# Kernel optimization log

Measured on AMD Instinct MI355X. Metric: run time of the kernel, lower is better.

## Reference

```python
import jax, jax.numpy as jnp
import numpy as np
from jax import lax

# dims
B, T = 64, 1024
ANNOT, RNN, MEM, ATTN = 512, 1024, 512, 512
FILTERS, KSIZE = 32, 31
PAD = (KSIZE - 1) // 2  # 15, SAME padding


def setup_inputs() -> dict:
    key = jax.random.key(0)
    ks = jax.random.split(key, 20)
    s = 0.02
    return {
        "memory": jax.random.normal(ks[0], (B, MEM), jnp.float32),
        "context": jax.random.normal(ks[1], (B, ANNOT), jnp.float32),
        "rnn_state": jax.random.normal(ks[2], (B, RNN), jnp.float32),
        "annots": jax.random.normal(ks[3], (B, T, ANNOT), jnp.float32),
        "atten": jax.random.uniform(ks[4], (B, 2, T), jnp.float32),
        "mask": jnp.ones((B, T), jnp.int32),
        "t": 0,
        # GRUCell params (torch gate order: r, z, n)
        "W_ih": jax.random.normal(ks[5], (3 * RNN, ANNOT + MEM), jnp.float32) * s,
        "W_hh": jax.random.normal(ks[6], (3 * RNN, RNN), jnp.float32) * s,
        "b_ih": jnp.zeros((3 * RNN,), jnp.float32),
        "b_hh": jnp.zeros((3 * RNN,), jnp.float32),
        # location-sensitive attention params
        "conv_w": jax.random.normal(ks[7], (FILTERS, 2, KSIZE), jnp.float32) * s,
        "loc_w": jax.random.normal(ks[8], (ATTN, FILTERS), jnp.float32) * s,
        "loc_b": jnp.zeros((ATTN,), jnp.float32),
        "q_w": jax.random.normal(ks[9], (ATTN, RNN), jnp.float32) * s,
        "q_b": jnp.zeros((ATTN,), jnp.float32),
        "a_w": jax.random.normal(ks[10], (ATTN, ANNOT), jnp.float32) * s,
        "a_b": jnp.zeros((ATTN,), jnp.float32),
        "v_w": jax.random.normal(ks[11], (1, ATTN), jnp.float32) * s,
    }


def _gru_cell(x, h, W_ih, W_hh, b_ih, b_hh):
    gi = x @ W_ih.T + b_ih  # [B, 3H]
    gh = h @ W_hh.T + b_hh
    i_r, i_z, i_n = jnp.split(gi, 3, axis=-1)
    h_r, h_z, h_n = jnp.split(gh, 3, axis=-1)
    r = jax.nn.sigmoid(i_r + h_r)
    z = jax.nn.sigmoid(i_z + h_z)
    n = jnp.tanh(i_n + r * h_n)
    return (1.0 - z) * n + z * h


def reference(memory, context, rnn_state, annots, atten, mask, t,
              W_ih, W_hh, b_ih, b_hh, conv_w, loc_w, loc_b,
              q_w, q_b, a_w, a_b, v_w):
    # GRU step on [memory; prev_context]
    rnn_input = jnp.concatenate([memory, context], axis=-1)  # [B, MEM+ANNOT]
    rnn_output = _gru_cell(rnn_input, rnn_state, W_ih, W_hh, b_ih, b_hh)  # [B, RNN]

    # location features: SAME conv over [B, 2, T] -> [B, FILTERS, T]
    loc_conv = lax.conv_general_dilated(
        atten, conv_w, window_strides=(1,), padding=[(PAD, PAD)],
        dimension_numbers=("NCH", "OIH", "NCH"))
    processed_loc = jnp.einsum("bft,af->bta", loc_conv, loc_w) + loc_b  # [B,T,ATTN]

    processed_query = (rnn_output @ q_w.T + q_b)[:, None, :]            # [B,1,ATTN]
    processed_annots = jnp.einsum("btd,ad->bta", annots, a_w) + a_b     # [B,T,ATTN]

    energy = jnp.tanh(processed_query + processed_annots + processed_loc)
    alignment = jnp.einsum("bta,a->bt", energy, v_w[0])                 # [B,T]

    # mask fill with -inf where mask == 0
    alignment = jnp.where(mask == 0, -jnp.inf, alignment)

    # sigmoid-normalized attention weights
    sig = jax.nn.sigmoid(alignment)
    alignment = sig / jnp.sum(sig, axis=1, keepdims=True)               # [B,T]

    new_context = jnp.einsum("bt,btd->bd", alignment, annots)           # [B,ANNOT]
    return rnn_output, new_context, alignment
```

## Files before the change

kernel.cpp:

```cpp
#include <hip/hip_runtime.h>

typedef float f32x4 __attribute__((ext_vector_type(4)));
typedef short bf16x8 __attribute__((ext_vector_type(8)));

__device__ __forceinline__ unsigned int pk2(float a, float b) {
    unsigned int ua = __float_as_uint(a); ua += 0x7FFFu + ((ua >> 16) & 1u);
    unsigned int ub = __float_as_uint(b); ub += 0x7FFFu + ((ub >> 16) & 1u);
    return __builtin_amdgcn_perm(ub, ua, 0x07060302u);
}
__device__ __forceinline__ unsigned short bf16_rne(float a) {
    unsigned int ua = __float_as_uint(a);
    ua += 0x7FFFu + ((ua >> 16) & 1u);
    return (unsigned short)(ua >> 16);
}
__device__ __forceinline__ float tanh_fast(float x) {
    float e = __expf(x + x);
    return 1.f - 2.f / (e + 1.f);
}
__device__ __forceinline__ f32x4 mfma16(bf16x8 a, bf16x8 b, f32x4 c) {
    return __builtin_amdgcn_mfma_f32_16x16x32_bf16(a, b, c, 0, 0, 0);
}
__device__ __forceinline__ void ald16(const void* g, void* l) {
    __builtin_amdgcn_global_load_lds(
        (const __attribute__((address_space(1))) unsigned int*)g,
        (__attribute__((address_space(3))) unsigned int*)l, 16, 0, 0);
}

#define Q_WIH   786432
#define Q_WHH   1572864
#define Q_QW    1703936
#define Q_X2    1720320
#define Q_X1    1736704
#define Q_BAW   1802240
#define Q_BLW   1806336
#define Q_EB    1806464
#define NCVT    7057

__global__ __launch_bounds__(256) void k_prep(
    const float* __restrict__ Wih, const float* __restrict__ Whh,
    const float* __restrict__ qw, const float* __restrict__ rnn_state,
    const float* __restrict__ memory, const float* __restrict__ context,
    const float* __restrict__ aw, const float* __restrict__ lw,
    const float* __restrict__ ab, const float* __restrict__ lb,
    const float* __restrict__ atten, const float* __restrict__ convw,
    unsigned short* __restrict__ Wihb, unsigned short* __restrict__ Whhb,
    unsigned short* __restrict__ qwb, unsigned short* __restrict__ X2b,
    unsigned short* __restrict__ X1b, unsigned short* __restrict__ Bbig,
    float* __restrict__ ebias, unsigned short* __restrict__ Lconv)
{
    __shared__ float att_s[2 * 160];
    __shared__ float cw_s[1984];
    const int tid = threadIdx.x;
    if (blockIdx.x < NCVT) {
        int q = blockIdx.x * 256 + tid;
        if (q >= Q_EB) return;
        if (q < Q_WIH) {
            int i = q * 4;
            float4 v = *(const float4*)(Wih + i);
            uint2 u; u.x = pk2(v.x, v.y); u.y = pk2(v.z, v.w);
            *(uint2*)(Wihb + i) = u;
        } else if (q < Q_WHH) {
            int i = (q - Q_WIH) * 4;
            float4 v = *(const float4*)(Whh + i);
            uint2 u; u.x = pk2(v.x, v.y); u.y = pk2(v.z, v.w);
            *(uint2*)(Whhb + i) = u;
        } else if (q < Q_QW) {
            int i = (q - Q_WHH) * 4;
            float4 v = *(const float4*)(qw + i);
            uint2 u; u.x = pk2(v.x, v.y); u.y = pk2(v.z, v.w);
            *(uint2*)(qwb + i) = u;
        } else if (q < Q_X2) {
            int i = (q - Q_QW) * 4;
            float4 v = *(const float4*)(rnn_state + i);
            uint2 u; u.x = pk2(v.x, v.y); u.y = pk2(v.z, v.w);
            *(uint2*)(X2b + i) = u;
        } else if (q < Q_X1) {
            int i = (q - Q_X2) * 4;
            int b = i >> 10, c = i & 1023;
            const float* s = (c < 512) ? (memory + b * 512 + c) : (context + b * 512 + (c - 512));
            float4 v = *(const float4*)s;
            uint2 u; u.x = pk2(v.x, v.y); u.y = pk2(v.z, v.w);
            *(uint2*)(X1b + i) = u;
        } else if (q < Q_BAW) {
            int i = (q - Q_X1) * 4;
            int a = i >> 9, c = i & 511;
            float4 v = *(const float4*)(aw + a * 512 + c);
            uint2 u; u.x = pk2(v.x, v.y); u.y = pk2(v.z, v.w);
            *(uint2*)(Bbig + a * 544 + c) = u;
        } else if (q < Q_BLW) {
            int i = (q - Q_BAW) * 4;
            int a = i >> 5, c = i & 31;
            float4 v = *(const float4*)(lw + a * 32 + c);
            uint2 u; u.x = pk2(v.x, v.y); u.y = pk2(v.z, v.w);
            *(uint2*)(Bbig + a * 544 + 512 + c) = u;
        } else {
            int i = (q - Q_BLW) * 4;
            float4 va = *(const float4*)(ab + i);
            float4 vb = *(const float4*)(lb + i);
            float4 r; r.x = va.x + vb.x; r.y = va.y + vb.y; r.z = va.z + vb.z; r.w = va.w + vb.w;
            *(float4*)(ebias + i) = r;
        }
    } else {
        const int bid = blockIdx.x - NCVT;
        const int b = bid >> 3;
        const int tbase = (bid & 7) * 128;
        for (int i = tid; i < 320; i += 256) {
            int c = i / 160, j = i % 160;
            float v = 0.f;
            int pos = tbase - 15 + j;
            if (j < 158 && pos >= 0 && pos < 1024) v = atten[b * 2048 + c * 1024 + pos];
            att_s[c * 160 + j] = v;
        }
        for (int i = tid; i < 1984; i += 256) cw_s[i] = convw[i];
        __syncthreads();
        const int f = tid & 31, tq = tid >> 5;
        float acc[16];
#pragma unroll
        for (int i = 0; i < 16; ++i) acc[i] = 0.f;
        for (int c = 0; c < 2; ++c) {
            for (int k = 0; k < 31; ++k) {
                float w = cw_s[f * 62 + c * 31 + k];
                int base = c * 160 + tq * 16 + k;
#pragma unroll
                for (int ti = 0; ti < 16; ++ti) acc[ti] += w * att_s[base + ti];
            }
        }
#pragma unroll
        for (int ti = 0; ti < 16; ++ti) {
            int t = tbase + tq * 16 + ti;
            Lconv[(b * 1024 + t) * 32 + f] = bf16_rne(acc[ti]);
        }
    }
}

__global__ __launch_bounds__(256, 4) void k_gemm_ks(
    const unsigned short* __restrict__ A1, const unsigned short* __restrict__ A2,
    const unsigned short* __restrict__ B1, const unsigned short* __restrict__ B2,
    float* __restrict__ C, int N, int nTiles, int n_split, int K, int Klen)
{
    __shared__ __align__(16) unsigned short As[64 * 32];
    __shared__ __align__(16) unsigned short Bs[128 * 32];
    const int tid = threadIdx.x;
    const int nb = blockIdx.x % nTiles;
    const int ks = blockIdx.x / nTiles;
    const int nBase = nb * 128;
    const bool use2 = nBase >= n_split;
    const unsigned short* A = use2 ? A2 : A1;
    const unsigned short* B = use2 ? B2 : B1;
    const int brow0 = nBase - (use2 ? n_split : 0);
    const int lane = tid & 63, w = tid >> 6;
    const int c = lane & 15, qd = lane >> 4;
    const int lr = lane >> 2;
    const int swzl = ((lane & 3) ^ ((lr >> 1) & 3)) * 8;

    const f32x4 fz = {0.f, 0.f, 0.f, 0.f};
    f32x4 acc[4][2];
#pragma unroll
    for (int i = 0; i < 4; ++i) { acc[i][0] = fz; acc[i][1] = fz; }

    const int k0b = ks * Klen;
    const int nkc = Klen >> 5;
    for (int kc = 0; kc < nkc; ++kc) {
        const int k0 = k0b + kc * 32;
        ald16(A + (size_t)(w * 16 + lr) * K + k0 + swzl, &As[w * 512]);
        ald16(B + (size_t)(brow0 + w * 16 + lr) * K + k0 + swzl, &Bs[w * 512]);
        ald16(B + (size_t)(brow0 + 64 + w * 16 + lr) * K + k0 + swzl, &Bs[2048 + w * 512]);
        __syncthreads();
        const int rdoff = (qd ^ ((c >> 1) & 3)) * 8;
        bf16x8 af[4];
#pragma unroll
        for (int i = 0; i < 4; ++i) af[i] = *(const bf16x8*)&As[(i * 16 + c) * 32 + rdoff];
#pragma unroll
        for (int j = 0; j < 2; ++j) {
            bf16x8 bj = *(const bf16x8*)&Bs[(w * 32 + j * 16 + c) * 32 + rdoff];
#pragma unroll
            for (int i = 0; i < 4; ++i) acc[i][j] = mfma16(af[i], bj, acc[i][j]);
        }
        __syncthreads();
    }
    float* Cp = C + (size_t)ks * 64 * N;
#pragma unroll
    for (int i = 0; i < 4; ++i)
#pragma unroll
        for (int r = 0; r < 4; ++r) {
            int row = i * 16 + qd * 4 + r;
#pragma unroll
            for (int j = 0; j < 2; ++j) {
                int col = nBase + w * 32 + j * 16 + c;
                Cp[row * N + col] = acc[i][j][r];
            }
        }
}

__global__ __launch_bounds__(256) void k_gates(
    const float* __restrict__ Cg, const float* __restrict__ h0,
    const float* __restrict__ bih, const float* __restrict__ bhh,
    float* __restrict__ outv, unsigned short* __restrict__ X3b)
{
    int idx = blockIdx.x * 256 + threadIdx.x;
    int b = idx >> 10, h = idx & 1023;
    const float* g0 = Cg + b * 6144;
    const float* g1 = Cg + 393216 + b * 6144;
    float ir = g0[h] + g1[h] + bih[h];
    float iz = g0[h + 1024] + g1[h + 1024] + bih[h + 1024];
    float inn = g0[h + 2048] + g1[h + 2048] + bih[h + 2048];
    float hr = g0[h + 3072] + g1[h + 3072] + bhh[h];
    float hz = g0[h + 4096] + g1[h + 4096] + bhh[h + 1024];
    float hn = g0[h + 5120] + g1[h + 5120] + bhh[h + 2048];
    float r = 1.f / (1.f + __expf(-(ir + hr)));
    float z = 1.f / (1.f + __expf(-(iz + hz)));
    float n = tanh_fast(inn + r * hn);
    float o = (1.f - z) * n + z * h0[idx];
    outv[idx] = o;
    X3b[idx] = bf16_rne(o);
}

__global__ __launch_bounds__(256, 2) void k_attn(
    const float* __restrict__ annots, const unsigned short* __restrict__ Lconv,
    const unsigned short* __restrict__ Bbig, const float* __restrict__ pqP,
    const float* __restrict__ qb, const float* __restrict__ ebias,
    const float* __restrict__ vw, float* __restrict__ wsal)
{
    __shared__ __align__(16) unsigned short As[64 * 32];
    __shared__ __align__(16) unsigned short Bs[512 * 32];
    __shared__ float red[4][64];
    const int tid = threadIdx.x;
    const int btBase = blockIdx.x * 64;
    const int b = btBase >> 10;
    const int lane = tid & 63, w = tid >> 6;
    const int c = lane & 15, qd = lane >> 4;
    const int lr = lane >> 2;
    const int swzl = ((lane & 3) ^ ((lr >> 1) & 3)) * 8;
    const int arow = tid >> 2, alc = tid & 3;
    const int apofs = (alc ^ ((arow >> 1) & 3)) * 8;

    const f32x4 fz = {0.f, 0.f, 0.f, 0.f};
    f32x4 acc[4][8];
#pragma unroll
    for (int i = 0; i < 4; ++i)
#pragma unroll
        for (int j = 0; j < 8; ++j) acc[i][j] = fz;

    for (int kc = 0; kc < 17; ++kc) {
        const int k0 = kc * 32;
#pragma unroll
        for (int s = 0; s < 8; ++s)
            ald16(Bbig + (size_t)(s * 64 + w * 16 + lr) * 544 + k0 + swzl,
                  &Bs[s * 2048 + w * 512]);
        if (kc < 16) {
            const float* p = annots + (size_t)(btBase + arow) * 512 + k0 + alc * 8;
            float4 v0 = *(const float4*)p;
            float4 v1 = *(const float4*)(p + 4);
            uint4 u;
            u.x = pk2(v0.x, v0.y); u.y = pk2(v0.z, v0.w);
            u.z = pk2(v1.x, v1.y); u.w = pk2(v1.z, v1.w);
            *(uint4*)&As[arow * 32 + apofs] = u;
        } else {
            ald16(Lconv + (size_t)(btBase + w * 16 + lr) * 32 + swzl, &As[w * 512]);
        }
        __syncthreads();
        const int rdoff = (qd ^ ((c >> 1) & 3)) * 8;
        bf16x8 af[4];
#pragma unroll
        for (int i = 0; i < 4; ++i) af[i] = *(const bf16x8*)&As[(i * 16 + c) * 32 + rdoff];
#pragma unroll
        for (int j = 0; j < 8; ++j) {
            bf16x8 bj = *(const bf16x8*)&Bs[(w * 128 + j * 16 + c) * 32 + rdoff];
#pragma unroll
            for (int i = 0; i < 4; ++i) acc[i][j] = mfma16(af[i], bj, acc[i][j]);
        }
        __syncthreads();
    }
    float pe[8], vv[8];
#pragma unroll
    for (int j = 0; j < 8; ++j) {
        int colg = w * 128 + j * 16 + c;
        pe[j] = pqP[b * 512 + colg] + pqP[32768 + b * 512 + colg] + qb[colg] + ebias[colg];
        vv[j] = vw[colg];
    }
#pragma unroll
    for (int i = 0; i < 4; ++i)
#pragma unroll
        for (int r = 0; r < 4; ++r) {
            float p = 0.f;
#pragma unroll
            for (int j = 0; j < 8; ++j)
                p += vv[j] * tanh_fast(acc[i][j][r] + pe[j]);
            p += __shfl_xor(p, 1);
            p += __shfl_xor(p, 2);
            p += __shfl_xor(p, 4);
            p += __shfl_xor(p, 8);
            if (c == 0) red[w][i * 16 + qd * 4 + r] = p;
        }
    __syncthreads();
    if (tid < 64)
        wsal[btBase + tid] = red[0][tid] + red[1][tid] + red[2][tid] + red[3][tid];
}

__global__ __launch_bounds__(256) void k_ctx(
    const float* __restrict__ annots, const float* __restrict__ wsal,
    const int* __restrict__ mask, float* __restrict__ out)
{
    __shared__ float al[1024];
    __shared__ float wsum[4];
    __shared__ float red[256];
    const int b = blockIdx.x >> 3;
    const int chunk = blockIdx.x & 7;
    const int tid = threadIdx.x;
    float lsum = 0.f;
#pragma unroll
    for (int p = 0; p < 4; ++p) {
        int t = p * 256 + tid;
        int bt = b * 1024 + t;
        float raw = wsal[bt];
        float s = (mask[bt] != 0) ? 1.f / (1.f + __expf(-raw)) : 0.f;
        al[t] = s;
        lsum += s;
    }
    for (int off = 32; off > 0; off >>= 1) lsum += __shfl_xor(lsum, off);
    if ((tid & 63) == 0) wsum[tid >> 6] = lsum;
    __syncthreads();
    const float tot = wsum[0] + wsum[1] + wsum[2] + wsum[3];
    const float inv = 1.f / tot;
    if (chunk == 0) {
#pragma unroll
        for (int p = 0; p < 4; ++p) {
            int t = p * 256 + tid;
            out[98304 + b * 1024 + t] = al[t] * inv;
        }
    }
    const int dq = tid & 63, tq = tid >> 6;
    const int d = chunk * 64 + dq;
    const float* ap = annots + (size_t)(b * 1024 + tq * 256) * 512 + d;
    float acc = 0.f;
#pragma unroll 4
    for (int t = 0; t < 256; ++t) acc += al[tq * 256 + t] * ap[(size_t)t * 512];
    red[tid] = acc;
    __syncthreads();
    if (tid < 64) {
        float s2 = red[tid] + red[64 + tid] + red[128 + tid] + red[192 + tid];
        out[65536 + b * 512 + chunk * 64 + tid] = s2 * inv;
    }
}

extern "C" void kernel_launch(void* const* d_in, const int* in_sizes, int n_in,
                              void* d_out, int out_size, void* d_ws, size_t ws_size,
                              hipStream_t stream) {
    const float* memory    = (const float*)d_in[0];
    const float* context   = (const float*)d_in[1];
    const float* rnn_state = (const float*)d_in[2];
    const float* annots    = (const float*)d_in[3];
    const float* atten     = (const float*)d_in[4];
    const int*   mask      = (const int*)d_in[5];
    const float* W_ih   = (const float*)d_in[7];
    const float* W_hh   = (const float*)d_in[8];
    const float* b_ih   = (const float*)d_in[9];
    const float* b_hh   = (const float*)d_in[10];
    const float* conv_w = (const float*)d_in[11];
    const float* loc_w  = (const float*)d_in[12];
    const float* loc_b  = (const float*)d_in[13];
    const float* q_w    = (const float*)d_in[14];
    const float* q_b    = (const float*)d_in[15];
    const float* a_w    = (const float*)d_in[16];
    const float* a_b    = (const float*)d_in[17];
    const float* v_w    = (const float*)d_in[18];
    float* out = (float*)d_out;

    char* w8 = (char*)d_ws;
    unsigned short* Lconv = (unsigned short*)(w8 + 0);
    unsigned short* Bbig  = (unsigned short*)(w8 + 4194304);
    unsigned short* Wihb  = (unsigned short*)(w8 + 4751360);
    unsigned short* Whhb  = (unsigned short*)(w8 + 11042816);
    unsigned short* qwb   = (unsigned short*)(w8 + 17334272);
    unsigned short* X1b   = (unsigned short*)(w8 + 18382848);
    unsigned short* X2b   = (unsigned short*)(w8 + 18513920);
    unsigned short* X3b   = (unsigned short*)(w8 + 18644992);
    float*          Cgru  = (float*)(w8 + 18776064);
    float*          pqP   = (float*)(w8 + 18776064);
    float*          wsal  = (float*)(w8 + 19038208);
    float*          ebias = (float*)(w8 + 21921792);

    k_prep<<<NCVT + 512, 256, 0, stream>>>(W_ih, W_hh, q_w, rnn_state, memory, context,
                                           a_w, loc_w, a_b, loc_b, atten, conv_w,
                                           Wihb, Whhb, qwb, X2b, X1b, Bbig, ebias, Lconv);
    k_gemm_ks<<<96, 256, 0, stream>>>(X1b, X2b, Wihb, Whhb, Cgru, 6144, 48, 3072, 1024, 512);
    k_gates<<<256, 256, 0, stream>>>(Cgru, rnn_state, b_ih, b_hh, out, X3b);
    k_gemm_ks<<<8, 256, 0, stream>>>(X3b, X3b, qwb, qwb, pqP, 512, 4, 0x40000000, 1024, 512);
    k_attn<<<1024, 256, 0, stream>>>(annots, Lconv, Bbig, pqP, q_b, ebias, v_w, wsal);
    k_ctx<<<512, 256, 0, stream>>>(annots, wsal, mask, out);
}
```

Baseline: 345.8 us.

## Pre-convert annots to bf16, split attention N across blocks, deepen GEMM K-split

Adds a bf16 conversion of the full annots tensor in the prep kernel and makes the attention and context kernels read that copy instead of fp32. The attention kernel now splits the 512 attention columns over two blocks, each with half the LDS and accumulators and a higher occupancy bound, and loads A tiles with async global-to-LDS copies. The two partial scores are summed in k_ctx. The GRU and query GEMMs use a 4-way K split with twice the blocks, so k_gates and k_attn now sum four partials. The cost is an extra full pass over annots (read fp32, write bf16) and bf16 rounding in the context sum.

```diff
diff --git a/kernel.cpp b/kernel.cpp
--- a/kernel.cpp
+++ b/kernel.cpp
@@ -13,6 +13,9 @@
     ua += 0x7FFFu + ((ua >> 16) & 1u);
     return (unsigned short)(ua >> 16);
 }
+__device__ __forceinline__ float bf2f(unsigned int us) {
+    return __uint_as_float(us << 16);
+}
 __device__ __forceinline__ float tanh_fast(float x) {
     float e = __expf(x + x);
     return 1.f - 2.f / (e + 1.f);
@@ -26,6 +29,7 @@
         (__attribute__((address_space(3))) unsigned int*)l, 16, 0, 0);
 }
 
+#define NB_ANN  16384
 #define Q_WIH   786432
 #define Q_WHH   1572864
 #define Q_QW    1703936
@@ -34,9 +38,11 @@
 #define Q_BAW   1802240
 #define Q_BLW   1806336
 #define Q_EB    1806464
-#define NCVT    7057
+#define NB_CVT  7057
+#define NB_PREP (NB_ANN + NB_CVT + 512)
 
 __global__ __launch_bounds__(256) void k_prep(
+    const float* __restrict__ annots, unsigned short* __restrict__ annb,
     const float* __restrict__ Wih, const float* __restrict__ Whh,
     const float* __restrict__ qw, const float* __restrict__ rnn_state,
     const float* __restrict__ memory, const float* __restrict__ context,
@@ -51,8 +57,16 @@
     __shared__ float att_s[2 * 160];
     __shared__ float cw_s[1984];
     const int tid = threadIdx.x;
-    if (blockIdx.x < NCVT) {
-        int q = blockIdx.x * 256 + tid;
+    if (blockIdx.x < NB_ANN) {
+        size_t i = ((size_t)blockIdx.x * 256 + tid) * 8;
+        float4 v0 = *(const float4*)(annots + i);
+        float4 v1 = *(const float4*)(annots + i + 4);
+        uint4 u;
+        u.x = pk2(v0.x, v0.y); u.y = pk2(v0.z, v0.w);
+        u.z = pk2(v1.x, v1.y); u.w = pk2(v1.z, v1.w);
+        *(uint4*)(annb + i) = u;
+    } else if (blockIdx.x < NB_ANN + NB_CVT) {
+        int q = (blockIdx.x - NB_ANN) * 256 + tid;
         if (q >= Q_EB) return;
         if (q < Q_WIH) {
             int i = q * 4;
@@ -101,7 +115,7 @@
             *(float4*)(ebias + i) = r;
         }
     } else {
-        const int bid = blockIdx.x - NCVT;
+        const int bid = blockIdx.x - (NB_ANN + NB_CVT);
         const int b = bid >> 3;
         const int tbase = (bid & 7) * 128;
         for (int i = tid; i < 320; i += 256) {
@@ -199,14 +213,17 @@
 {
     int idx = blockIdx.x * 256 + threadIdx.x;
     int b = idx >> 10, h = idx & 1023;
-    const float* g0 = Cg + b * 6144;
-    const float* g1 = Cg + 393216 + b * 6144;
-    float ir = g0[h] + g1[h] + bih[h];
-    float iz = g0[h + 1024] + g1[h + 1024] + bih[h + 1024];
-    float inn = g0[h + 2048] + g1[h + 2048] + bih[h + 2048];
-    float hr = g0[h + 3072] + g1[h + 3072] + bhh[h];
-    float hz = g0[h + 4096] + g1[h + 4096] + bhh[h + 1024];
-    float hn = g0[h + 5120] + g1[h + 5120] + bhh[h + 2048];
+    float s[6];
+#pragma unroll
+    for (int g = 0; g < 6; ++g) s[g] = 0.f;
+#pragma unroll
+    for (int ks = 0; ks < 4; ++ks) {
+        const float* g = Cg + ks * 393216 + b * 6144 + h;
+#pragma unroll
+        for (int k = 0; k < 6; ++k) s[k] += g[k * 1024];
+    }
+    float ir = s[0] + bih[h], iz = s[1] + bih[h + 1024], inn = s[2] + bih[h + 2048];
+    float hr = s[3] + bhh[h], hz = s[4] + bhh[h + 1024], hn = s[5] + bhh[h + 2048];
     float r = 1.f / (1.f + __expf(-(ir + hr)));
     float z = 1.f / (1.f + __expf(-(iz + hz)));
     float n = tanh_fast(inn + r * hn);
@@ -215,67 +232,65 @@
     X3b[idx] = bf16_rne(o);
 }
 
-__global__ __launch_bounds__(256, 2) void k_attn(
-    const float* __restrict__ annots, const unsigned short* __restrict__ Lconv,
+__global__ __launch_bounds__(256, 4) void k_attn(
+    const unsigned short* __restrict__ annb, const unsigned short* __restrict__ Lconv,
     const unsigned short* __restrict__ Bbig, const float* __restrict__ pqP,
     const float* __restrict__ qb, const float* __restrict__ ebias,
     const float* __restrict__ vw, float* __restrict__ wsal)
 {
     __shared__ __align__(16) unsigned short As[64 * 32];
-    __shared__ __align__(16) unsigned short Bs[512 * 32];
+    __shared__ __align__(16) unsigned short Bs[256 * 32];
     __shared__ float red[4][64];
     const int tid = threadIdx.x;
-    const int btBase = blockIdx.x * 64;
-    const int b = btBase >> 10;
+    const int mtile = blockIdx.x >> 1;
+    const int split = blockIdx.x & 1;
+    const int btBase = mtile * 64;
+    const int b = mtile >> 4;
+    const int nb2 = split * 256;
     const int lane = tid & 63, w = tid >> 6;
     const int c = lane & 15, qd = lane >> 4;
     const int lr = lane >> 2;
     const int swzl = ((lane & 3) ^ ((lr >> 1) & 3)) * 8;
-    const int arow = tid >> 2, alc = tid & 3;
-    const int apofs = (alc ^ ((arow >> 1) & 3)) * 8;
 
     const f32x4 fz = {0.f, 0.f, 0.f, 0.f};
-    f32x4 acc[4][8];
+    f32x4 acc[4][4];
 #pragma unroll
     for (int i = 0; i < 4; ++i)
 #pragma unroll
-        for (int j = 0; j < 8; ++j) acc[i][j] = fz;
-
+        for (int j = 0; j < 4; ++j) acc[i][j] = fz;
+
+    const int arow = btBase + w * 16 + lr;
     for (int kc = 0; kc < 17; ++kc) {
         const int k0 = kc * 32;
-#pragma unroll
-        for (int s = 0; s < 8; ++s)
-            ald16(Bbig + (size_t)(s * 64 + w * 16 + lr) * 544 + k0 + swzl,
+        if (kc < 16)
+            ald16(annb + (size_t)arow * 512 + k0 + swzl, &As[w * 512]);
+        else
+            ald16(Lconv + (size_t)arow * 32 + swzl, &As[w * 512]);
+#pragma unroll
+        for (int s = 0; s < 4; ++s)
+            ald16(Bbig + (size_t)(nb2 + s * 64 + w * 16 + lr) * 544 + k0 + swzl,
                   &Bs[s * 2048 + w * 512]);
-        if (kc < 16) {
-            const float* p = annots + (size_t)(btBase + arow) * 512 + k0 + alc * 8;
-            float4 v0 = *(const float4*)p;
-            float4 v1 = *(const float4*)(p + 4);
-            uint4 u;
-            u.x = pk2(v0.x, v0.y); u.y = pk2(v0.z, v0.w);
-            u.z = pk2(v1.x, v1.y); u.w = pk2(v1.z, v1.w);
-            *(uint4*)&As[arow * 32 + apofs] = u;
-        } else {
-            ald16(Lconv + (size_t)(btBase + w * 16 + lr) * 32 + swzl, &As[w * 512]);
-        }
         __syncthreads();
         const int rdoff = (qd ^ ((c >> 1) & 3)) * 8;
         bf16x8 af[4];
 #pragma unroll
         for (int i = 0; i < 4; ++i) af[i] = *(const bf16x8*)&As[(i * 16 + c) * 32 + rdoff];
 #pragma unroll
-        for (int j = 0; j < 8; ++j) {
-            bf16x8 bj = *(const bf16x8*)&Bs[(w * 128 + j * 16 + c) * 32 + rdoff];
+        for (int j = 0; j < 4; ++j) {
+            bf16x8 bj = *(const bf16x8*)&Bs[(w * 64 + j * 16 + c) * 32 + rdoff];
 #pragma unroll
             for (int i = 0; i < 4; ++i) acc[i][j] = mfma16(af[i], bj, acc[i][j]);
         }
         __syncthreads();
     }
-    float pe[8], vv[8];
-#pragma unroll
-    for (int j = 0; j < 8; ++j) {
-        int colg = w * 128 + j * 16 + c;
-        pe[j] = pqP[b * 512 + colg] + pqP[32768 + b * 512 + colg] + qb[colg] + ebias[colg];
+    float pe[4], vv[4];
+#pragma unroll
+    for (int j = 0; j < 4; ++j) {
+        int colg = nb2 + w * 64 + j * 16 + c;
+        float pq = qb[colg] + ebias[colg];
+#pragma unroll
+        for (int ks = 0; ks < 4; ++ks) pq += pqP[ks * 32768 + b * 512 + colg];
+        pe[j] = pq;
         vv[j] = vw[colg];
     }
 #pragma unroll
@@ -284,7 +299,7 @@
         for (int r = 0; r < 4; ++r) {
             float p = 0.f;
 #pragma unroll
-            for (int j = 0; j < 8; ++j)
+            for (int j = 0; j < 4; ++j)
                 p += vv[j] * tanh_fast(acc[i][j][r] + pe[j]);
             p += __shfl_xor(p, 1);
             p += __shfl_xor(p, 2);
@@ -294,25 +309,25 @@
         }
     __syncthreads();
     if (tid < 64)
-        wsal[btBase + tid] = red[0][tid] + red[1][tid] + red[2][tid] + red[3][tid];
+        wsal[split * 65536 + btBase + tid] = red[0][tid] + red[1][tid] + red[2][tid] + red[3][tid];
 }
 
 __global__ __launch_bounds__(256) void k_ctx(
-    const float* __restrict__ annots, const float* __restrict__ wsal,
+    const unsigned short* __restrict__ annb, const float* __restrict__ wsal,
     const int* __restrict__ mask, float* __restrict__ out)
 {
     __shared__ float al[1024];
     __shared__ float wsum[4];
-    __shared__ float red[256];
-    const int b = blockIdx.x >> 3;
-    const int chunk = blockIdx.x & 7;
+    __shared__ float2 red[256];
+    const int b = blockIdx.x >> 2;
+    const int chunk = blockIdx.x & 3;
     const int tid = threadIdx.x;
     float lsum = 0.f;
 #pragma unroll
     for (int p = 0; p < 4; ++p) {
         int t = p * 256 + tid;
         int bt = b * 1024 + t;
-        float raw = wsal[bt];
+        float raw = wsal[bt] + wsal[65536 + bt];
         float s = (mask[bt] != 0) ? 1.f / (1.f + __expf(-raw)) : 0.f;
         al[t] = s;
         lsum += s;
@@ -330,16 +345,24 @@
         }
     }
     const int dq = tid & 63, tq = tid >> 6;
-    const int d = chunk * 64 + dq;
-    const float* ap = annots + (size_t)(b * 1024 + tq * 256) * 512 + d;
-    float acc = 0.f;
+    const int d0 = chunk * 128 + dq * 2;
+    const unsigned short* ap = annb + (size_t)(b * 1024 + tq * 256) * 512 + d0;
+    float a0 = 0.f, a1 = 0.f;
 #pragma unroll 4
-    for (int t = 0; t < 256; ++t) acc += al[tq * 256 + t] * ap[(size_t)t * 512];
-    red[tid] = acc;
+    for (int t = 0; t < 256; ++t) {
+        unsigned int u = *(const unsigned int*)(ap + (size_t)t * 512);
+        float wgt = al[tq * 256 + t];
+        a0 += wgt * bf2f(u & 0xFFFFu);
+        a1 += wgt * bf2f(u >> 16);
+    }
+    red[tid].x = a0; red[tid].y = a1;
     __syncthreads();
     if (tid < 64) {
-        float s2 = red[tid] + red[64 + tid] + red[128 + tid] + red[192 + tid];
-        out[65536 + b * 512 + chunk * 64 + tid] = s2 * inv;
+        float2 s2;
+        s2.x = red[tid].x + red[64 + tid].x + red[128 + tid].x + red[192 + tid].x;
+        s2.y = red[tid].y + red[64 + tid].y + red[128 + tid].y + red[192 + tid].y;
+        float2 o; o.x = s2.x * inv; o.y = s2.y * inv;
+        *(float2*)(out + 65536 + b * 512 + chunk * 128 + tid * 2) = o;
     }
 }
 
@@ -369,23 +392,25 @@
     char* w8 = (char*)d_ws;
     unsigned short* Lconv = (unsigned short*)(w8 + 0);
     unsigned short* Bbig  = (unsigned short*)(w8 + 4194304);
-    unsigned short* Wihb  = (unsigned short*)(w8 + 4751360);
-    unsigned short* Whhb  = (unsigned short*)(w8 + 11042816);
-    unsigned short* qwb   = (unsigned short*)(w8 + 17334272);
-    unsigned short* X1b   = (unsigned short*)(w8 + 18382848);
-    unsigned short* X2b   = (unsigned short*)(w8 + 18513920);
-    unsigned short* X3b   = (unsigned short*)(w8 + 18644992);
-    float*          Cgru  = (float*)(w8 + 18776064);
-    float*          pqP   = (float*)(w8 + 18776064);
-    float*          wsal  = (float*)(w8 + 19038208);
-    float*          ebias = (float*)(w8 + 21921792);
-
-    k_prep<<<NCVT + 512, 256, 0, stream>>>(W_ih, W_hh, q_w, rnn_state, memory, context,
-                                           a_w, loc_w, a_b, loc_b, atten, conv_w,
-                                           Wihb, Whhb, qwb, X2b, X1b, Bbig, ebias, Lconv);
-    k_gemm_ks<<<96, 256, 0, stream>>>(X1b, X2b, Wihb, Whhb, Cgru, 6144, 48, 3072, 1024, 512);
+    unsigned short* annb  = (unsigned short*)(w8 + 4751360);
+    unsigned short* Wihb  = (unsigned short*)(w8 + 71860224);
+    unsigned short* Whhb  = (unsigned short*)(w8 + 78151680);
+    unsigned short* qwb   = (unsigned short*)(w8 + 84443136);
+    unsigned short* X1b   = (unsigned short*)(w8 + 85491712);
+    unsigned short* X2b   = (unsigned short*)(w8 + 85622784);
+    unsigned short* X3b   = (unsigned short*)(w8 + 85753856);
+    float*          Cgru  = (float*)(w8 + 85884928);
+    float*          pqP   = (float*)(w8 + 92176384);
+    float*          wsal  = (float*)(w8 + 92700672);
+    float*          ebias = (float*)(w8 + 93224960);
+
+    k_prep<<<NB_PREP, 256, 0, stream>>>(annots, annb,
+                                        W_ih, W_hh, q_w, rnn_state, memory, context,
+                                        a_w, loc_w, a_b, loc_b, atten, conv_w,
+                                        Wihb, Whhb, qwb, X2b, X1b, Bbig, ebias, Lconv);
+    k_gemm_ks<<<192, 256, 0, stream>>>(X1b, X2b, Wihb, Whhb, Cgru, 6144, 48, 3072, 1024, 256);
     k_gates<<<256, 256, 0, stream>>>(Cgru, rnn_state, b_ih, b_hh, out, X3b);
-    k_gemm_ks<<<8, 256, 0, stream>>>(X3b, X3b, qwb, qwb, pqP, 512, 4, 0x40000000, 1024, 512);
-    k_attn<<<1024, 256, 0, stream>>>(annots, Lconv, Bbig, pqP, q_b, ebias, v_w, wsal);
-    k_ctx<<<512, 256, 0, stream>>>(annots, wsal, mask, out);
-}
+    k_gemm_ks<<<16, 256, 0, stream>>>(X3b, X3b, qwb, qwb, pqP, 512, 4, 0x40000000, 1024, 256);
+    k_attn<<<2048, 256, 0, stream>>>(annb, Lconv, Bbig, pqP, q_b, ebias, v_w, wsal);
+    k_ctx<<<256, 256, 0, stream>>>(annb, wsal, mask, out);
+}
```

Measured after the change: 362.5 us. 4.8% more time.

## Split attention N dimension and deepen split-K in GRU and query GEMMs

Applied to the files above, without the earlier changes.

The attention kernel now splits the 512 attention columns across two blocks. Each block stages only half of B in LDS, keeps fewer accumulators and allows four blocks per CU, and the two partial alignment sums are added in the context kernel. The GRU and query GEMMs double their split-K factor (K chunk 256 instead of 512), so they launch twice as many blocks, and the gates and attention kernels sum four partials. This raises parallelism and occupancy on small grids, at the cost of re-reading and re-converting annots twice in k_attn and of extra partial-sum traffic.

```diff
diff --git a/kernel.cpp b/kernel.cpp
--- a/kernel.cpp
+++ b/kernel.cpp
@@ -34,7 +34,7 @@
 #define Q_BAW   1802240
 #define Q_BLW   1806336
 #define Q_EB    1806464
-#define NCVT    7057
+#define NB_CVT  7057
 
 __global__ __launch_bounds__(256) void k_prep(
     const float* __restrict__ Wih, const float* __restrict__ Whh,
@@ -51,7 +51,7 @@
     __shared__ float att_s[2 * 160];
     __shared__ float cw_s[1984];
     const int tid = threadIdx.x;
-    if (blockIdx.x < NCVT) {
+    if (blockIdx.x < NB_CVT) {
         int q = blockIdx.x * 256 + tid;
         if (q >= Q_EB) return;
         if (q < Q_WIH) {
@@ -101,7 +101,7 @@
             *(float4*)(ebias + i) = r;
         }
     } else {
-        const int bid = blockIdx.x - NCVT;
+        const int bid = blockIdx.x - NB_CVT;
         const int b = bid >> 3;
         const int tbase = (bid & 7) * 128;
         for (int i = tid; i < 320; i += 256) {
@@ -199,14 +199,17 @@
 {
     int idx = blockIdx.x * 256 + threadIdx.x;
     int b = idx >> 10, h = idx & 1023;
-    const float* g0 = Cg + b * 6144;
-    const float* g1 = Cg + 393216 + b * 6144;
-    float ir = g0[h] + g1[h] + bih[h];
-    float iz = g0[h + 1024] + g1[h + 1024] + bih[h + 1024];
-    float inn = g0[h + 2048] + g1[h + 2048] + bih[h + 2048];
-    float hr = g0[h + 3072] + g1[h + 3072] + bhh[h];
-    float hz = g0[h + 4096] + g1[h + 4096] + bhh[h + 1024];
-    float hn = g0[h + 5120] + g1[h + 5120] + bhh[h + 2048];
+    float s[6];
+#pragma unroll
+    for (int g = 0; g < 6; ++g) s[g] = 0.f;
+#pragma unroll
+    for (int ks = 0; ks < 4; ++ks) {
+        const float* g = Cg + ks * 393216 + b * 6144 + h;
+#pragma unroll
+        for (int k = 0; k < 6; ++k) s[k] += g[k * 1024];
+    }
+    float ir = s[0] + bih[h], iz = s[1] + bih[h + 1024], inn = s[2] + bih[h + 2048];
+    float hr = s[3] + bhh[h], hz = s[4] + bhh[h + 1024], hn = s[5] + bhh[h + 2048];
     float r = 1.f / (1.f + __expf(-(ir + hr)));
     float z = 1.f / (1.f + __expf(-(iz + hz)));
     float n = tanh_fast(inn + r * hn);
@@ -215,18 +218,21 @@
     X3b[idx] = bf16_rne(o);
 }
 
-__global__ __launch_bounds__(256, 2) void k_attn(
+__global__ __launch_bounds__(256, 4) void k_attn(
     const float* __restrict__ annots, const unsigned short* __restrict__ Lconv,
     const unsigned short* __restrict__ Bbig, const float* __restrict__ pqP,
     const float* __restrict__ qb, const float* __restrict__ ebias,
     const float* __restrict__ vw, float* __restrict__ wsal)
 {
     __shared__ __align__(16) unsigned short As[64 * 32];
-    __shared__ __align__(16) unsigned short Bs[512 * 32];
+    __shared__ __align__(16) unsigned short Bs[256 * 32];
     __shared__ float red[4][64];
     const int tid = threadIdx.x;
-    const int btBase = blockIdx.x * 64;
-    const int b = btBase >> 10;
+    const int mtile = blockIdx.x >> 1;
+    const int split = blockIdx.x & 1;
+    const int btBase = mtile * 64;
+    const int b = mtile >> 4;
+    const int nb2 = split * 256;
     const int lane = tid & 63, w = tid >> 6;
     const int c = lane & 15, qd = lane >> 4;
     const int lr = lane >> 2;
@@ -235,17 +241,17 @@
     const int apofs = (alc ^ ((arow >> 1) & 3)) * 8;
 
     const f32x4 fz = {0.f, 0.f, 0.f, 0.f};
-    f32x4 acc[4][8];
+    f32x4 acc[4][4];
 #pragma unroll
     for (int i = 0; i < 4; ++i)
 #pragma unroll
-        for (int j = 0; j < 8; ++j) acc[i][j] = fz;
+        for (int j = 0; j < 4; ++j) acc[i][j] = fz;
 
     for (int kc = 0; kc < 17; ++kc) {
         const int k0 = kc * 32;
 #pragma unroll
-        for (int s = 0; s < 8; ++s)
-            ald16(Bbig + (size_t)(s * 64 + w * 16 + lr) * 544 + k0 + swzl,
+        for (int s = 0; s < 4; ++s)
+            ald16(Bbig + (size_t)(nb2 + s * 64 + w * 16 + lr) * 544 + k0 + swzl,
                   &Bs[s * 2048 + w * 512]);
         if (kc < 16) {
             const float* p = annots + (size_t)(btBase + arow) * 512 + k0 + alc * 8;
@@ -264,18 +270,21 @@
 #pragma unroll
         for (int i = 0; i < 4; ++i) af[i] = *(const bf16x8*)&As[(i * 16 + c) * 32 + rdoff];
 #pragma unroll
-        for (int j = 0; j < 8; ++j) {
-            bf16x8 bj = *(const bf16x8*)&Bs[(w * 128 + j * 16 + c) * 32 + rdoff];
+        for (int j = 0; j < 4; ++j) {
+            bf16x8 bj = *(const bf16x8*)&Bs[(w * 64 + j * 16 + c) * 32 + rdoff];
 #pragma unroll
             for (int i = 0; i < 4; ++i) acc[i][j] = mfma16(af[i], bj, acc[i][j]);
         }
         __syncthreads();
     }
-    float pe[8], vv[8];
-#pragma unroll
-    for (int j = 0; j < 8; ++j) {
-        int colg = w * 128 + j * 16 + c;
-        pe[j] = pqP[b * 512 + colg] + pqP[32768 + b * 512 + colg] + qb[colg] + ebias[colg];
+    float pe[4], vv[4];
+#pragma unroll
+    for (int j = 0; j < 4; ++j) {
+        int colg = nb2 + w * 64 + j * 16 + c;
+        float pq = qb[colg] + ebias[colg];
+#pragma unroll
+        for (int ks = 0; ks < 4; ++ks) pq += pqP[ks * 32768 + b * 512 + colg];
+        pe[j] = pq;
         vv[j] = vw[colg];
     }
 #pragma unroll
@@ -284,7 +293,7 @@
         for (int r = 0; r < 4; ++r) {
             float p = 0.f;
 #pragma unroll
-            for (int j = 0; j < 8; ++j)
+            for (int j = 0; j < 4; ++j)
                 p += vv[j] * tanh_fast(acc[i][j][r] + pe[j]);
             p += __shfl_xor(p, 1);
             p += __shfl_xor(p, 2);
@@ -294,7 +303,7 @@
         }
     __syncthreads();
     if (tid < 64)
-        wsal[btBase + tid] = red[0][tid] + red[1][tid] + red[2][tid] + red[3][tid];
+        wsal[split * 65536 + btBase + tid] = red[0][tid] + red[1][tid] + red[2][tid] + red[3][tid];
 }
 
 __global__ __launch_bounds__(256) void k_ctx(
@@ -312,7 +321,7 @@
     for (int p = 0; p < 4; ++p) {
         int t = p * 256 + tid;
         int bt = b * 1024 + t;
-        float raw = wsal[bt];
+        float raw = wsal[bt] + wsal[65536 + bt];
         float s = (mask[bt] != 0) ? 1.f / (1.f + __expf(-raw)) : 0.f;
         al[t] = s;
         lsum += s;
@@ -376,16 +385,16 @@
     unsigned short* X2b   = (unsigned short*)(w8 + 18513920);
     unsigned short* X3b   = (unsigned short*)(w8 + 18644992);
     float*          Cgru  = (float*)(w8 + 18776064);
-    float*          pqP   = (float*)(w8 + 18776064);
-    float*          wsal  = (float*)(w8 + 19038208);
-    float*          ebias = (float*)(w8 + 21921792);
-
-    k_prep<<<NCVT + 512, 256, 0, stream>>>(W_ih, W_hh, q_w, rnn_state, memory, context,
-                                           a_w, loc_w, a_b, loc_b, atten, conv_w,
-                                           Wihb, Whhb, qwb, X2b, X1b, Bbig, ebias, Lconv);
-    k_gemm_ks<<<96, 256, 0, stream>>>(X1b, X2b, Wihb, Whhb, Cgru, 6144, 48, 3072, 1024, 512);
+    float*          pqP   = (float*)(w8 + 25067520);
+    float*          wsal  = (float*)(w8 + 25591808);
+    float*          ebias = (float*)(w8 + 26116096);
+
+    k_prep<<<NB_CVT + 512, 256, 0, stream>>>(W_ih, W_hh, q_w, rnn_state, memory, context,
+                                             a_w, loc_w, a_b, loc_b, atten, conv_w,
+                                             Wihb, Whhb, qwb, X2b, X1b, Bbig, ebias, Lconv);
+    k_gemm_ks<<<192, 256, 0, stream>>>(X1b, X2b, Wihb, Whhb, Cgru, 6144, 48, 3072, 1024, 256);
     k_gates<<<256, 256, 0, stream>>>(Cgru, rnn_state, b_ih, b_hh, out, X3b);
-    k_gemm_ks<<<8, 256, 0, stream>>>(X3b, X3b, qwb, qwb, pqP, 512, 4, 0x40000000, 1024, 512);
-    k_attn<<<1024, 256, 0, stream>>>(annots, Lconv, Bbig, pqP, q_b, ebias, v_w, wsal);
+    k_gemm_ks<<<16, 256, 0, stream>>>(X3b, X3b, qwb, qwb, pqP, 512, 4, 0x40000000, 1024, 256);
+    k_attn<<<2048, 256, 0, stream>>>(annots, Lconv, Bbig, pqP, q_b, ebias, v_w, wsal);
     k_ctx<<<512, 256, 0, stream>>>(annots, wsal, mask, out);
 }
```

After: 353.0 us. 2.1% more time.
